# Kernel optimization log

Hardware: AMD Instinct MI355X
Metric: run time of the kernel (lower is better)

Reference implementation:

```python
import jax, jax.numpy as jnp
import numpy as np

N_RAYS = 65536
N_SAMPLES = 96


def setup_inputs() -> dict:
    key = jax.random.key(0)
    k1, k2, k3 = jax.random.split(key, 3)
    rgb = jax.random.uniform(k1, (N_RAYS, N_SAMPLES, 3), dtype=jnp.float32)
    # SDF values near the surface, small magnitude
    sdf = jax.random.normal(k2, (N_RAYS, N_SAMPLES), dtype=jnp.float32) * 0.1
    # monotonically increasing sample depths along each ray
    z_vals = jnp.sort(
        jax.random.uniform(k3, (N_RAYS, N_SAMPLES), dtype=jnp.float32,
                           minval=0.1, maxval=5.0), axis=-1)
    return {"rgb": rgb, "sdf": sdf, "z_vals": z_vals, "beta": 10}


def reference(rgb, sdf, z_vals, beta):
    # sdf2alpha: alpha = 1 - exp(-beta * sigmoid(-sdf * beta))
    alpha = 1.0 - jnp.exp(-beta * jax.nn.sigmoid(-sdf * beta))  # [N, S]
    # exclusive cumprod of (1 - alpha + 1e-10): transmittance
    trans = jnp.cumprod(
        jnp.concatenate([jnp.ones_like(alpha[:, :1]), 1.0 - alpha + 1e-10],
                        axis=-1), axis=-1)[:, :-1]  # [N, S]
    weights = alpha * trans  # [N, S]
    rendered_rgb = jnp.sum(weights[..., None] * rgb, axis=-2)  # [N, 3]
    rendered_depth = jnp.sum(weights * z_vals, axis=-1)  # [N]
    return (rendered_depth, rendered_rgb, sdf, z_vals)
```

## Files before the change

kernel.cpp:

```cpp
#include <hip/hip_runtime.h>


#define SDFR_NS 96
#define SDFR_NCOPY 2048

struct f3 { float x, y, z; };
typedef float fv4 __attribute__((ext_vector_type(4)));

__global__ __launch_bounds__(256, 8) void sdf_render_kernel(
    const float* __restrict__ rgb,
    const float* __restrict__ sdf,
    const float* __restrict__ z_vals,
    const int*   __restrict__ beta_p,
    float* __restrict__ out_depth,
    float* __restrict__ out_rgb,
    float* __restrict__ out_sdf,
    float* __restrict__ out_z,
    int n_rays)
{
    const int t = threadIdx.x;

    if (blockIdx.x < SDFR_NCOPY) {
        const int n4 = (n_rays * SDFR_NS) / 4;
        const int stride = SDFR_NCOPY * 256;
        const fv4* __restrict__ s4 = (const fv4*)sdf;
        const fv4* __restrict__ z4 = (const fv4*)z_vals;
        fv4* __restrict__ os4 = (fv4*)out_sdf;
        fv4* __restrict__ oz4 = (fv4*)out_z;

        for (int i = blockIdx.x * 256 + t; i < n4; i += stride) {
            const fv4 a = s4[i];
            const fv4 b = z4[i];
            __builtin_nontemporal_store(a, os4 + i);
            __builtin_nontemporal_store(b, oz4 + i);
        }
        return;
    }

    const int cbid = blockIdx.x - SDFR_NCOPY;
    const int tid  = cbid * 256 + t;
    const int ray  = tid >> 5;
    const int l    = tid & 31;
    if (ray >= n_rays) return;

    const int sb = ray * SDFR_NS + 3 * l;
    const int rb = ray * (SDFR_NS * 3) + 9 * l;

    const f3 sv = *(const f3*)(sdf    + sb);
    const f3 zv = *(const f3*)(z_vals + sb);
    const f3 ca = *(const f3*)(rgb + rb + 0);
    const f3 cb = *(const f3*)(rgb + rb + 3);
    const f3 cc = *(const f3*)(rgb + rb + 6);
    __builtin_amdgcn_sched_barrier(0);

    int bi = *beta_p;
    float beta;
    if (bi > 1000000 || bi < -1000000) {
        union { int i; float f; } u; u.i = bi; beta = u.f;
    } else {
        beta = (float)bi;
    }

    const float e0 = __expf(-beta * __builtin_amdgcn_rcpf(1.0f + __expf(sv.x * beta)));
    const float e1 = __expf(-beta * __builtin_amdgcn_rcpf(1.0f + __expf(sv.y * beta)));
    const float e2 = __expf(-beta * __builtin_amdgcn_rcpf(1.0f + __expf(sv.z * beta)));
    const float a0 = 1.0f - e0, t0 = e0 + 1e-10f;
    const float a1 = 1.0f - e1, t1 = e1 + 1e-10f;
    const float a2 = 1.0f - e2, t2 = e2 + 1e-10f;

    const float m = t0 * t1 * t2;
    float scan = m;
    #pragma unroll
    for (int d = 1; d < 32; d <<= 1) {
        float v = __shfl_up(scan, d, 32);
        if (l >= d) scan *= v;
    }
    float E = __shfl_up(scan, 1, 32);
    if (l == 0) E = 1.0f;

    const float w0 = a0 * E;
    const float w1 = a1 * E * t0;
    const float w2 = a2 * E * t0 * t1;

    float depth = w0 * zv.x + w1 * zv.y + w2 * zv.z;
    float r0    = w0 * ca.x + w1 * cb.x + w2 * cc.x;
    float r1    = w0 * ca.y + w1 * cb.y + w2 * cc.y;
    float r2    = w0 * ca.z + w1 * cb.z + w2 * cc.z;

    #pragma unroll
    for (int d = 16; d >= 1; d >>= 1) {
        depth += __shfl_xor(depth, d, 32);
        r0    += __shfl_xor(r0, d, 32);
        r1    += __shfl_xor(r1, d, 32);
        r2    += __shfl_xor(r2, d, 32);
    }

    if (l == 0) {
        out_depth[ray] = depth;
        f3 o; o.x = r0; o.y = r1; o.z = r2;
        *(f3*)(out_rgb + ray * 3) = o;
    }
}

extern "C" void kernel_launch(void* const* d_in, const int* in_sizes, int n_in,
                              void* d_out, int out_size, void* d_ws, size_t ws_size,
                              hipStream_t stream) {
    (void)n_in; (void)d_ws; (void)ws_size; (void)out_size;

    const float* rgb    = (const float*)d_in[0];
    const float* sdf    = (const float*)d_in[1];
    const float* z      = (const float*)d_in[2];
    const int*   beta_p = (const int*)d_in[3];

    const int n_rays = in_sizes[1] / SDFR_NS;

    float* out_depth = (float*)d_out;
    float* out_rgb   = out_depth + n_rays;
    float* out_sdf   = out_rgb   + (size_t)n_rays * 3;
    float* out_z     = out_sdf   + (size_t)n_rays * SDFR_NS;

    const int comp_blocks = (n_rays * 32 + 255) / 256;
    const int grid = SDFR_NCOPY + comp_blocks;
    sdf_render_kernel<<<grid, 256, 0, stream>>>(
        rgb, sdf, z, beta_p, out_depth, out_rgb, out_sdf, out_z, n_rays);
}
```

Before: 164.7 us.

## Interleave copy and compute blocks, process four rays per warp with prefetch

Replaces the separate copy-then-compute block ranges with even/odd interleaved blocks over a fixed grid. Copy blocks issue three vec4 loads per array before storing, and compute blocks handle 32 rays each, double-buffering loads of the next ray while computing the current one. The aim is more memory-level parallelism and less block launch overhead, at the cost of more registers (launch bounds lowered to 6) and a grid that no longer scales with n_rays beyond 65536.

```diff
diff --git a/kernel.cpp b/kernel.cpp
--- a/kernel.cpp
+++ b/kernel.cpp
@@ -2,65 +2,16 @@
 
 
 #define SDFR_NS 96
-#define SDFR_NCOPY 2048
+#define SDFR_HALF 2048
 
 struct f3 { float x, y, z; };
 typedef float fv4 __attribute__((ext_vector_type(4)));
 
-__global__ __launch_bounds__(256, 8) void sdf_render_kernel(
-    const float* __restrict__ rgb,
-    const float* __restrict__ sdf,
-    const float* __restrict__ z_vals,
-    const int*   __restrict__ beta_p,
-    float* __restrict__ out_depth,
-    float* __restrict__ out_rgb,
-    float* __restrict__ out_sdf,
-    float* __restrict__ out_z,
-    int n_rays)
+__device__ __forceinline__ void compute_ray(
+    int l, float beta,
+    const f3& sv, const f3& zv, const f3& ca, const f3& cb, const f3& cc,
+    float& depth, float& r0, float& r1, float& r2)
 {
-    const int t = threadIdx.x;
-
-    if (blockIdx.x < SDFR_NCOPY) {
-        const int n4 = (n_rays * SDFR_NS) / 4;
-        const int stride = SDFR_NCOPY * 256;
-        const fv4* __restrict__ s4 = (const fv4*)sdf;
-        const fv4* __restrict__ z4 = (const fv4*)z_vals;
-        fv4* __restrict__ os4 = (fv4*)out_sdf;
-        fv4* __restrict__ oz4 = (fv4*)out_z;
-
-        for (int i = blockIdx.x * 256 + t; i < n4; i += stride) {
-            const fv4 a = s4[i];
-            const fv4 b = z4[i];
-            __builtin_nontemporal_store(a, os4 + i);
-            __builtin_nontemporal_store(b, oz4 + i);
-        }
-        return;
-    }
-
-    const int cbid = blockIdx.x - SDFR_NCOPY;
-    const int tid  = cbid * 256 + t;
-    const int ray  = tid >> 5;
-    const int l    = tid & 31;
-    if (ray >= n_rays) return;
-
-    const int sb = ray * SDFR_NS + 3 * l;
-    const int rb = ray * (SDFR_NS * 3) + 9 * l;
-
-    const f3 sv = *(const f3*)(sdf    + sb);
-    const f3 zv = *(const f3*)(z_vals + sb);
-    const f3 ca = *(const f3*)(rgb + rb + 0);
-    const f3 cb = *(const f3*)(rgb + rb + 3);
-    const f3 cc = *(const f3*)(rgb + rb + 6);
-    __builtin_amdgcn_sched_barrier(0);
-
-    int bi = *beta_p;
-    float beta;
-    if (bi > 1000000 || bi < -1000000) {
-        union { int i; float f; } u; u.i = bi; beta = u.f;
-    } else {
-        beta = (float)bi;
-    }
-
     const float e0 = __expf(-beta * __builtin_amdgcn_rcpf(1.0f + __expf(sv.x * beta)));
     const float e1 = __expf(-beta * __builtin_amdgcn_rcpf(1.0f + __expf(sv.y * beta)));
     const float e2 = __expf(-beta * __builtin_amdgcn_rcpf(1.0f + __expf(sv.z * beta)));
@@ -68,8 +19,7 @@
     const float a1 = 1.0f - e1, t1 = e1 + 1e-10f;
     const float a2 = 1.0f - e2, t2 = e2 + 1e-10f;
 
-    const float m = t0 * t1 * t2;
-    float scan = m;
+    float scan = t0 * t1 * t2;
     #pragma unroll
     for (int d = 1; d < 32; d <<= 1) {
         float v = __shfl_up(scan, d, 32);
@@ -82,10 +32,10 @@
     const float w1 = a1 * E * t0;
     const float w2 = a2 * E * t0 * t1;
 
-    float depth = w0 * zv.x + w1 * zv.y + w2 * zv.z;
-    float r0    = w0 * ca.x + w1 * cb.x + w2 * cc.x;
-    float r1    = w0 * ca.y + w1 * cb.y + w2 * cc.y;
-    float r2    = w0 * ca.z + w1 * cb.z + w2 * cc.z;
+    depth = w0 * zv.x + w1 * zv.y + w2 * zv.z;
+    r0    = w0 * ca.x + w1 * cb.x + w2 * cc.x;
+    r1    = w0 * ca.y + w1 * cb.y + w2 * cc.y;
+    r2    = w0 * ca.z + w1 * cb.z + w2 * cc.z;
 
     #pragma unroll
     for (int d = 16; d >= 1; d >>= 1) {
@@ -94,12 +44,132 @@
         r1    += __shfl_xor(r1, d, 32);
         r2    += __shfl_xor(r2, d, 32);
     }
+}
 
-    if (l == 0) {
-        out_depth[ray] = depth;
-        f3 o; o.x = r0; o.y = r1; o.z = r2;
-        *(f3*)(out_rgb + ray * 3) = o;
+__global__ __launch_bounds__(256, 6) void sdf_render_kernel(
+    const float* __restrict__ rgb,
+    const float* __restrict__ sdf,
+    const float* __restrict__ z_vals,
+    const int*   __restrict__ beta_p,
+    float* __restrict__ out_depth,
+    float* __restrict__ out_rgb,
+    float* __restrict__ out_sdf,
+    float* __restrict__ out_z,
+    int n_rays)
+{
+    const int t    = threadIdx.x;
+    const int half = blockIdx.x >> 1;
+
+    if ((blockIdx.x & 1) == 0) {
+        const int n4     = (n_rays * SDFR_NS) / 4;
+        const int stride = SDFR_HALF * 256;
+        const int i0 = half * 256 + t;
+        const int i1 = i0 + stride;
+        const int i2 = i0 + 2 * stride;
+        const fv4* __restrict__ s4 = (const fv4*)sdf;
+        const fv4* __restrict__ z4 = (const fv4*)z_vals;
+        fv4* __restrict__ os4 = (fv4*)out_sdf;
+        fv4* __restrict__ oz4 = (fv4*)out_z;
+
+        if (i2 < n4) {
+            const fv4 a0 = s4[i0], a1 = s4[i1], a2 = s4[i2];
+            const fv4 b0 = z4[i0], b1 = z4[i1], b2 = z4[i2];
+            __builtin_amdgcn_sched_barrier(0);
+            __builtin_nontemporal_store(a0, os4 + i0);
+            __builtin_nontemporal_store(a1, os4 + i1);
+            __builtin_nontemporal_store(a2, os4 + i2);
+            __builtin_nontemporal_store(b0, oz4 + i0);
+            __builtin_nontemporal_store(b1, oz4 + i1);
+            __builtin_nontemporal_store(b2, oz4 + i2);
+        } else {
+            for (int i = i0; i < n4; i += stride) {
+                const fv4 a = s4[i];
+                const fv4 b = z4[i];
+                __builtin_nontemporal_store(a, os4 + i);
+                __builtin_nontemporal_store(b, oz4 + i);
+            }
+        }
+        return;
     }
+
+    const int g    = t >> 5;
+    const int l    = t & 31;
+    const int base = half * 32;
+
+    int bi = *beta_p;
+    float beta;
+    if (bi > 1000000 || bi < -1000000) {
+        union { int i; float f; } u; u.i = bi; beta = u.f;
+    } else {
+        beta = (float)bi;
+    }
+
+    f3 svA, zvA, caA, cbA, ccA;
+    f3 svB, zvB, caB, cbB, ccB;
+
+#define SDFR_LOAD(SFX, RAY)                                         \
+    do {                                                            \
+        const int sb_ = (RAY) * SDFR_NS + 3 * l;                    \
+        const int rb_ = (RAY) * (SDFR_NS * 3) + 9 * l;              \
+        sv##SFX = *(const f3*)(sdf    + sb_);                       \
+        zv##SFX = *(const f3*)(z_vals + sb_);                       \
+        ca##SFX = *(const f3*)(rgb + rb_ + 0);                      \
+        cb##SFX = *(const f3*)(rgb + rb_ + 3);                      \
+        cc##SFX = *(const f3*)(rgb + rb_ + 6);                      \
+    } while (0)
+
+#define SDFR_STORE(RAY, D, R0, R1, R2)                              \
+    do {                                                            \
+        if (l == 0) {                                               \
+            out_depth[(RAY)] = (D);                                 \
+            f3 o_; o_.x = (R0); o_.y = (R1); o_.z = (R2);           \
+            *(f3*)(out_rgb + (RAY) * 3) = o_;                       \
+        }                                                           \
+    } while (0)
+
+    if (base + 32 <= n_rays) {
+        const int r0_ = base +  0 + g;
+        const int r1_ = base +  8 + g;
+        const int r2_ = base + 16 + g;
+        const int r3_ = base + 24 + g;
+
+        SDFR_LOAD(A, r0_);
+        SDFR_LOAD(B, r1_);
+        __builtin_amdgcn_sched_barrier(0);
+
+        float d0, x0, y0, w0_;
+        compute_ray(l, beta, svA, zvA, caA, cbA, ccA, d0, x0, y0, w0_);
+        SDFR_LOAD(A, r2_);
+        SDFR_STORE(r0_, d0, x0, y0, w0_);
+        __builtin_amdgcn_sched_barrier(0);
+
+        float d1, x1, y1, w1_;
+        compute_ray(l, beta, svB, zvB, caB, cbB, ccB, d1, x1, y1, w1_);
+        SDFR_LOAD(B, r3_);
+        SDFR_STORE(r1_, d1, x1, y1, w1_);
+        __builtin_amdgcn_sched_barrier(0);
+
+        float d2, x2, y2, w2_;
+        compute_ray(l, beta, svA, zvA, caA, cbA, ccA, d2, x2, y2, w2_);
+        SDFR_STORE(r2_, d2, x2, y2, w2_);
+
+        float d3, x3, y3, w3_;
+        compute_ray(l, beta, svB, zvB, caB, cbB, ccB, d3, x3, y3, w3_);
+        SDFR_STORE(r3_, d3, x3, y3, w3_);
+    } else {
+        for (int p = 0; p < 4; ++p) {
+            const int ray = base + p * 8 + g;
+            if (ray < n_rays) {
+                SDFR_LOAD(A, ray);
+                float d_, x_, y_, w_;
+                compute_ray(l, beta, svA, zvA, caA, cbA, ccA, d_, x_, y_, w_);
+                SDFR_STORE(ray, d_, x_, y_, w_);
+            }
+        }
+    }
+
+#undef SDFR_LOAD
+#undef SDFR_STORE
 }
 
 extern "C" void kernel_launch(void* const* d_in, const int* in_sizes, int n_in,
@@ -119,8 +189,7 @@
     float* out_sdf   = out_rgb   + (size_t)n_rays * 3;
     float* out_z     = out_sdf   + (size_t)n_rays * SDFR_NS;
 
-    const int comp_blocks = (n_rays * 32 + 255) / 256;
-    const int grid = SDFR_NCOPY + comp_blocks;
+    const int grid = 2 * SDFR_HALF;
     sdf_render_kernel<<<grid, 256, 0, stream>>>(
         rgb, sdf, z, beta_p, out_depth, out_rgb, out_sdf, out_z, n_rays);
 }
```

After: 171.7 us. +4.2%, slower.
